# Performance work log

Hardware: AMD Instinct MI355X
Metric: run time of the kernel (lower is better)

## Reference

```python
import jax, jax.numpy as jnp
import numpy as np

B, S, D, H, EXP = 4, 2048, 768, 8, 4
HD = D // H  # head dim = 96
EPS = 1e-5


def layer_norm(x, g, b):
    mu = jnp.mean(x, axis=-1, keepdims=True)
    var = jnp.mean(jnp.square(x - mu), axis=-1, keepdims=True)
    return (x - mu) * jax.lax.rsqrt(var + EPS) * g + b


def setup_inputs() -> dict:
    key = jax.random.key(0)
    ks = jax.random.split(key, 16)
    s = 0.02
    f32 = jnp.float32
    x = jax.random.normal(ks[0], (B, S, D), f32)
    Wq = jax.random.normal(ks[1], (D, D), f32) * s
    bq = jnp.zeros((D,), f32)
    Wk = jax.random.normal(ks[2], (D, D), f32) * s
    bk = jnp.zeros((D,), f32)
    Wv = jax.random.normal(ks[3], (D, D), f32) * s
    bv = jnp.zeros((D,), f32)
    Wo = jax.random.normal(ks[4], (D, D), f32) * s
    bo = jnp.zeros((D,), f32)
    g1 = jnp.ones((D,), f32)
    be1 = jnp.zeros((D,), f32)
    W1 = jax.random.normal(ks[5], (D, D * EXP), f32) * s
    bf1 = jnp.zeros((D * EXP,), f32)
    W2 = jax.random.normal(ks[6], (D * EXP, D), f32) * s
    bf2 = jnp.zeros((D,), f32)
    g2 = jnp.ones((D,), f32)
    be2 = jnp.zeros((D,), f32)
    return dict(x=x, Wq=Wq, bq=bq, Wk=Wk, bk=bk, Wv=Wv, bv=bv, Wo=Wo, bo=bo,
                g1=g1, be1=be1, W1=W1, bf1=bf1, W2=W2, bf2=bf2, g2=g2, be2=be2)


def reference(x, Wq, bq, Wk, bk, Wv, bv, Wo, bo, g1, be1, W1, bf1, W2, bf2, g2, be2):
    scale = HD ** (-0.5)
    # multi-head attention (manual QK^T softmax V)
    q = (x @ Wq + bq).reshape(B, S, H, HD).transpose(0, 2, 1, 3)  # b H s c
    k = (x @ Wk + bk).reshape(B, S, H, HD).transpose(0, 2, 1, 3)
    v = (x @ Wv + bv).reshape(B, S, H, HD).transpose(0, 2, 1, 3)
    scores = jnp.einsum('bhqc,bhkc->bhqk', q, k) * scale
    attn = jax.nn.softmax(scores, axis=-1)
    o = jnp.einsum('bhqk,bhkc->bhqc', attn, v)
    o = o.transpose(0, 2, 1, 3).reshape(B, S, D)
    attn_out = o @ Wo + bo
    # residual + LN
    x1 = layer_norm(attn_out + x, g1, be1)
    # feed-forward with GELU
    h = jax.nn.gelu(x1 @ W1 + bf1)
    ffn_out = h @ W2 + bf2
    # residual + LN
    return layer_norm(ffn_out + x1, g2, be2)
```

## Files before the change

### kernel.cpp

```cpp
#include <hip/hip_runtime.h>
#include <hip/hip_bf16.h>
#include <math.h>
#include <stdint.h>

#define B_    4
#define S_    2048
#define D_    768
#define H_    8
#define HD_   96
#define EXPD_ 3072
#define MSZ   8192

#define QSCALE 0.14724439f
#define M0_    12.0f

typedef __bf16 bf16;
typedef __bf16 bf16x4 __attribute__((ext_vector_type(4)));
typedef __bf16 bf16x8 __attribute__((ext_vector_type(8)));
typedef float  f32x4  __attribute__((ext_vector_type(4)));
typedef float  f32x16 __attribute__((ext_vector_type(16)));

typedef __attribute__((address_space(1))) const uint32_t gu32;
typedef __attribute__((address_space(3))) uint32_t lu32;

__device__ __forceinline__ void async_copy16(const void* g, void* l) {
    __builtin_amdgcn_global_load_lds((gu32*)g, (lu32*)l, 16, 0, 0);
}

template<int N> __device__ __forceinline__ void vm_wait() {
    if constexpr (N == 0)      asm volatile("s_waitcnt vmcnt(0)" ::: "memory");
    else if constexpr (N == 3) asm volatile("s_waitcnt vmcnt(3)" ::: "memory");
    else if constexpr (N == 4) asm volatile("s_waitcnt vmcnt(4)" ::: "memory");
    else static_assert(N == 0 || N == 3 || N == 4, "unsupported vmcnt");
}

__device__ __forceinline__ float gelu_f(float x) {
    float x3 = x * x * x;
    return 0.5f * x * (1.0f + tanhf(0.7978845608028654f * (x + 0.044715f * x3)));
}

__device__ __forceinline__ bool sniff_f32(const void* p) {
    const bf16* pb = (const bf16*)p;
    float v = (float)pb[2 * (threadIdx.x & 63)];
    bool big = !(fabsf(v) < 1000.0f);
    return __any(big) != 0;
}

__device__ __forceinline__ float dynld(const void* p, size_t i, bool f32in) {
    return f32in ? ((const float*)p)[i] : (float)((const bf16*)p)[i];
}

__global__ __launch_bounds__(256) void cast_kernel(
    const void* __restrict__ src, bf16* __restrict__ dst)
{
    const bool f32in = sniff_f32(src);
    size_t i = ((size_t)blockIdx.x * 256 + threadIdx.x) * 8;
    if (f32in) {
        f32x4 a = *(const f32x4*)((const float*)src + i);
        f32x4 b = *(const f32x4*)((const float*)src + i + 4);
        bf16x8 r;
#pragma unroll
        for (int e = 0; e < 4; ++e) { r[e] = (bf16)a[e]; r[e + 4] = (bf16)b[e]; }
        *(bf16x8*)(dst + i) = r;
    } else {
        *(bf16x8*)(dst + i) = *(const bf16x8*)((const bf16*)src + i);
    }
}

#define MODE_QKV  0
#define MODE_RES  1
#define MODE_GELU 2

template<int MODE, bool ADYN, bool RESDYN, int BN>
__global__ __launch_bounds__(256) void gemm2_kernel(
    const void* __restrict__ A, const bf16* __restrict__ Bt,
    const void* __restrict__ b0, const void* __restrict__ b1, const void* __restrict__ b2,
    const void* __restrict__ res, bf16* __restrict__ out,
    int M, int N, int K, int lda, int ldb, int boff, int mstripe,
    const void* __restrict__ sniffp)
{
    constexpr int WN   = BN / 2;
    constexpr int NJ32 = WN / 32;
    constexpr int ABUF = 8192;
    constexpr int BBUF = BN * 64;
    constexpr int BUF  = ABUF + BBUF;
    constexpr int LPH  = 2 + BN / 64;
    __shared__ __align__(16) bf16 Sh[2 * BUF];

    const bool f32in = sniff_f32(sniffp);
    const int tid  = threadIdx.x;
    const int w    = tid >> 6;
    const int lane = tid & 63;
    const int l32  = lane & 31;
    const int kh   = lane >> 5;
    const int wr   = w >> 1, wc = w & 1;

    const int lin  = blockIdx.x;
    const int xcd  = lin & 7;
    const int q    = lin >> 3;
    const int nb   = q / mstripe;
    const int mbin = q - nb * mstripe;
    const int m0   = (xcd * mstripe + mbin) * 128;
    const int n0   = nb * BN;

    const int rsub = lane >> 2;
    const int cswz = (((lane & 3) ^ ((rsub >> 1) & 3))) * 8;
    const int xh   = (l32 >> 1) & 3;

    f32x16 acc[2][NJ32];
#pragma unroll
    for (int i = 0; i < 2; ++i)
#pragma unroll
        for (int j = 0; j < NJ32; ++j)
#pragma unroll
            for (int e = 0; e < 16; ++e) acc[i][j][e] = 0.f;

    const bf16*  Abf = (const bf16*)A;
    const float* Af  = (const float*)A;

    auto stage_half = [&](int k0, int h, int bsel) {
        bf16* As = Sh + bsel * BUF;
        bf16* Bs = As + ABUF;
#pragma unroll
        for (int a = 0; a < 2; ++a) {
            int row = w * 32 + a * 16 + rsub;
            async_copy16(Abf + (size_t)(m0 + row) * lda + k0 + h * 32 + cswz,
                         &As[h * 4096 + (w * 32 + a * 16) * 32]);
        }
#pragma unroll
        for (int a = 0; a < BN / 64; ++a) {
            int row = w * (BN / 4) + a * 16 + rsub;
            async_copy16(Bt + (size_t)(n0 + row) * ldb + k0 + h * 32 + cswz,
                         &Bs[h * (BN * 32) + (w * (BN / 4) + a * 16) * 32]);
        }
    };

    auto compute_half = [&](int hs, int bsel) {
        const bf16* As = Sh + bsel * BUF;
        const bf16* Bs = As + ABUF;
        bf16x8 af[2][2], bfv[NJ32][2];
#pragma unroll
        for (int i = 0; i < 2; ++i)
#pragma unroll
            for (int ks = 0; ks < 2; ++ks)
                af[i][ks] = *(const bf16x8*)(&As[hs * 4096 + (wr * 64 + i * 32 + l32) * 32
                                                + (((ks * 2 + kh) ^ xh) * 8)]);
#pragma unroll
        for (int j = 0; j < NJ32; ++j)
#pragma unroll
            for (int ks = 0; ks < 2; ++ks)
                bfv[j][ks] = *(const bf16x8*)(&Bs[hs * (BN * 32) + (wc * WN + j * 32 + l32) * 32
                                                  + (((ks * 2 + kh) ^ xh) * 8)]);
        asm volatile("s_waitcnt lgkmcnt(0)" ::: "memory");
        __builtin_amdgcn_sched_barrier(0);
        __builtin_amdgcn_s_setprio(1);
#pragma unroll
        for (int i = 0; i < 2; ++i)
#pragma unroll
            for (int j = 0; j < NJ32; ++j)
#pragma unroll
                for (int ks = 0; ks < 2; ++ks)
                    acc[i][j] = __builtin_amdgcn_mfma_f32_32x32x16_bf16(af[i][ks], bfv[j][ks], acc[i][j], 0, 0, 0);
        __builtin_amdgcn_s_setprio(0);
    };

    const int nk = K >> 6;
    if constexpr (ADYN) {
        auto stage = [&](int k0, int bsel) {
            bf16* As = Sh + bsel * BUF;
            bf16* Bs = As + ABUF;
#pragma unroll
            for (int half = 0; half < 2; ++half) {
                if (f32in) {
#pragma unroll
                    for (int a = 0; a < 2; ++a) {
                        const float* sp = Af + (size_t)(m0 + w * 32 + a * 16 + rsub) * lda + k0 + half * 32 + cswz;
                        f32x4 u0 = *(const f32x4*)sp;
                        f32x4 u1 = *(const f32x4*)(sp + 4);
                        bf16x8 v;
#pragma unroll
                        for (int e = 0; e < 4; ++e) { v[e] = (bf16)u0[e]; v[e + 4] = (bf16)u1[e]; }
                        *(bf16x8*)(&As[(size_t)(half * 4096) + (size_t)(w * 32 + a * 16) * 32 + lane * 8]) = v;
                    }
                } else {
#pragma unroll
                    for (int a = 0; a < 2; ++a) {
                        int row = w * 32 + a * 16 + rsub;
                        async_copy16(Abf + (size_t)(m0 + row) * lda + k0 + half * 32 + cswz,
                                     &As[half * 4096 + (w * 32 + a * 16) * 32]);
                    }
                }
#pragma unroll
                for (int a = 0; a < BN / 64; ++a) {
                    int row = w * (BN / 4) + a * 16 + rsub;
                    async_copy16(Bt + (size_t)(n0 + row) * ldb + k0 + half * 32 + cswz,
                                 &Bs[half * (BN * 32) + (w * (BN / 4) + a * 16) * 32]);
                }
            }
        };
        stage(0, 0);
        __syncthreads();
        for (int t = 0; t < nk; ++t) {
            const int cur = t & 1;
            if (t + 1 < nk) stage((t + 1) << 6, cur ^ 1);
            compute_half(0, cur);
            compute_half(1, cur);
            __syncthreads();
        }
    } else {
        stage_half(0, 0, 0);
        stage_half(0, 1, 0);
        vm_wait<LPH>();
        __builtin_amdgcn_s_barrier();
        for (int t = 0; t < nk; ++t) {
            const int cur = t & 1;
            const bool pf = (t + 1 < nk);
#pragma unroll
            for (int h = 0; h < 2; ++h) {
                if (pf) stage_half((t + 1) << 6, h, cur ^ 1);
                compute_half(h, cur);
                if (pf) vm_wait<LPH>(); else vm_wait<0>();
                __builtin_amdgcn_s_barrier();
            }
        }
    }
    __syncthreads();

    if constexpr (MODE == MODE_QKV) {
        bf16* Cw = Sh + w * 2048;
        const int bb = (m0 + wr * 64) >> 11;
#pragma unroll
        for (int j = 0; j < NJ32; ++j) {
            int nbase = n0 + wc * WN + j * 32;
            int which = nbase / D_;
            int n2b   = nbase - which * D_;
            int h     = n2b / HD_;
            int hd0   = n2b - h * HD_;
            const void* bp = which == 0 ? b0 : (which == 1 ? b1 : b2);
            float bval = dynld(bp, n2b + l32, f32in);
            const int bh = bb * H_ + h;
#pragma unroll
            for (int i = 0; i < 2; ++i)
#pragma unroll
                for (int g = 0; g < 16; ++g) {
                    int rr = (g & 3) + 8 * (g >> 2) + 4 * kh;
                    float v = acc[i][j][g] + bval;
                    if (which == 0) v *= QSCALE;
                    Cw[(i * 32 + rr) * 32 + l32] = (bf16)v;
                }
            if (which < 2) {
#pragma unroll
                for (int pass = 0; pass < 4; ++pass) {
                    int row = pass * 16 + (lane >> 2);
                    int c8  = (lane & 3) * 8;
                    bf16x8 cv = *(const bf16x8*)&Cw[row * 32 + c8];
                    int ss = (m0 + wr * 64 + row) & (S_ - 1);
                    size_t dst = (size_t)which * (MSZ * D_) + ((size_t)bh * S_ + ss) * HD_ + hd0 + c8;
                    *(bf16x8*)&out[dst] = cv;
                }
            } else {
                int hd  = hd0 + l32;
                int ss0 = (m0 + wr * 64) & (S_ - 1);
                size_t rowb = (size_t)2 * (MSZ * D_) + ((size_t)bh * HD_ + hd) * S_ + ss0 + kh * 32;
#pragma unroll
                for (int oct = 0; oct < 4; ++oct) {
                    bf16x8 cv;
#pragma unroll
                    for (int e = 0; e < 8; ++e)
                        cv[e] = Cw[(kh * 32 + oct * 8 + e) * 32 + l32];
                    *(bf16x8*)&out[rowb + oct * 8] = cv;
                }
            }
        }
    } else {
        bf16* Cw = Sh + w * 2048;
        for (int j = 0; j < NJ32; ++j) {
            int nl = n0 + wc * WN + j * 32 + l32;
            float bval = boff >= 0 ? dynld(b0, boff + nl, f32in) : 0.f;
#pragma unroll
            for (int i = 0; i < 2; ++i)
#pragma unroll
                for (int g = 0; g < 16; ++g) {
                    int rr = (g & 3) + 8 * (g >> 2) + 4 * kh;
                    float v = acc[i][j][g] + bval;
                    if constexpr (MODE == MODE_GELU) v = gelu_f(v);
                    Cw[(i * 32 + rr) * 32 + l32] = (bf16)v;
                }
#pragma unroll
            for (int pass = 0; pass < 4; ++pass) {
                int row = pass * 16 + (lane >> 2);
                int cc  = (lane & 3) * 8;
                bf16x8 cv = *(const bf16x8*)&Cw[row * 32 + cc];
                int m = m0 + wr * 64 + row;
                int n = n0 + wc * WN + j * 32 + cc;
                size_t off = (size_t)m * N + n;
                if constexpr (MODE == MODE_RES) {
                    bf16x8 o;
                    if (RESDYN && f32in) {
                        f32x4 r0 = *(const f32x4*)((const float*)res + off);
                        f32x4 r1 = *(const f32x4*)((const float*)res + off + 4);
#pragma unroll
                        for (int e = 0; e < 4; ++e) {
                            o[e]     = (bf16)((float)cv[e] + r0[e]);
                            o[e + 4] = (bf16)((float)cv[e + 4] + r1[e]);
                        }
                    } else {
                        bf16x8 rv = *(const bf16x8*)((const bf16*)res + off);
#pragma unroll
                        for (int e = 0; e < 8; ++e) o[e] = (bf16)((float)cv[e] + (float)rv[e]);
                    }
                    *(bf16x8*)&out[off] = o;
                } else {
                    *(bf16x8*)&out[off] = cv;
                }
            }
        }
    }
}

__global__ __launch_bounds__(256, 2) void flash_kernel(
    const bf16* __restrict__ Q, const bf16* __restrict__ Kk,
    const bf16* __restrict__ Vt_g, bf16* __restrict__ ctx)
{
    __shared__ __align__(16) bf16 Ks[64][104];
    __shared__ __align__(16) bf16 Vs[96][72];
    __shared__ __align__(16) bf16 Ps[4][32][72];

    const int tid  = threadIdx.x;
    const int w    = tid >> 6;
    const int lane = tid & 63;
    const int quad = lane >> 4;
    const int l16  = lane & 15;
    const int bh   = blockIdx.x;
    const size_t base = (size_t)bh * S_ * HD_;
    const int q0   = blockIdx.y * 128 + w * 32;

    bf16x8 qf[2][3];
#pragma unroll
    for (int qs = 0; qs < 2; ++qs)
#pragma unroll
        for (int ch = 0; ch < 3; ++ch)
            qf[qs][ch] = *(const bf16x8*)(Q + base + (size_t)(q0 + qs * 16 + l16) * HD_ + ch * 32 + quad * 8);

    f32x4 oacc[2][6];
#pragma unroll
    for (int qs = 0; qs < 2; ++qs)
#pragma unroll
        for (int c = 0; c < 6; ++c) oacc[qs][c] = (f32x4){0.f, 0.f, 0.f, 0.f};
    float lsum[2] = {0.f, 0.f};

    int krow[3], kc8[3], vrow[3], vc8[3];
#pragma unroll
    for (int i = 0; i < 3; ++i) {
        int id = tid + i * 256;
        krow[i] = id / 12; kc8[i] = (id - krow[i] * 12) * 8;
        vrow[i] = id >> 3; vc8[i] = (id & 7) * 8;
    }

    bf16x8 kreg[3], vreg[3];
#pragma unroll
    for (int i = 0; i < 3; ++i) {
        kreg[i] = *(const bf16x8*)(Kk + base + (size_t)krow[i] * HD_ + kc8[i]);
        vreg[i] = *(const bf16x8*)(Vt_g + base + (size_t)vrow[i] * S_ + vc8[i]);
    }
#pragma unroll
    for (int i = 0; i < 3; ++i) {
        *(bf16x8*)(&Ks[krow[i]][kc8[i]]) = kreg[i];
        *(bf16x8*)(&Vs[vrow[i]][vc8[i]]) = vreg[i];
    }
    __syncthreads();

    for (int kv0 = 0; kv0 < S_; kv0 += 64) {
        const bool more = (kv0 + 64) < S_;
        if (more) {
#pragma unroll
            for (int i = 0; i < 3; ++i) {
                kreg[i] = *(const bf16x8*)(Kk + base + (size_t)(kv0 + 64 + krow[i]) * HD_ + kc8[i]);
                vreg[i] = *(const bf16x8*)(Vt_g + base + (size_t)vrow[i] * S_ + kv0 + 64 + vc8[i]);
            }
        }

        f32x4 sacc[2][4];
#pragma unroll
        for (int qs = 0; qs < 2; ++qs)
#pragma unroll
            for (int t = 0; t < 4; ++t)
                sacc[qs][t] = (f32x4){-M0_, -M0_, -M0_, -M0_};
#pragma unroll
        for (int t = 0; t < 4; ++t)
#pragma unroll
            for (int ch = 0; ch < 3; ++ch) {
                bf16x8 kf = *(const bf16x8*)(&Ks[t * 16 + l16][ch * 32 + quad * 8]);
                sacc[0][t] = __builtin_amdgcn_mfma_f32_16x16x32_bf16(kf, qf[0][ch], sacc[0][t], 0, 0, 0);
                sacc[1][t] = __builtin_amdgcn_mfma_f32_16x16x32_bf16(kf, qf[1][ch], sacc[1][t], 0, 0, 0);
            }

#pragma unroll
        for (int qs = 0; qs < 2; ++qs) {
            bf16* prow = &Ps[w][qs * 16 + l16][quad * 4];
#pragma unroll
            for (int t = 0; t < 4; ++t) {
                float p0 = exp2f(sacc[qs][t][0]);
                float p1 = exp2f(sacc[qs][t][1]);
                float p2 = exp2f(sacc[qs][t][2]);
                float p3 = exp2f(sacc[qs][t][3]);
                lsum[qs] += (p0 + p1) + (p2 + p3);
                bf16x4 pv;
                pv[0] = (bf16)p0; pv[1] = (bf16)p1; pv[2] = (bf16)p2; pv[3] = (bf16)p3;
                *(bf16x4*)(prow + t * 16) = pv;
            }
        }

        bf16x8 pf[2][2];
#pragma unroll
        for (int qs = 0; qs < 2; ++qs) {
            pf[qs][0] = *(const bf16x8*)(&Ps[w][qs * 16 + l16][quad * 8]);
            pf[qs][1] = *(const bf16x8*)(&Ps[w][qs * 16 + l16][32 + quad * 8]);
        }
#pragma unroll
        for (int c = 0; c < 6; ++c) {
            bf16x8 vf0 = *(const bf16x8*)(&Vs[c * 16 + l16][quad * 8]);
            bf16x8 vf1 = *(const bf16x8*)(&Vs[c * 16 + l16][32 + quad * 8]);
            oacc[0][c] = __builtin_amdgcn_mfma_f32_16x16x32_bf16(pf[0][0], vf0, oacc[0][c], 0, 0, 0);
            oacc[0][c] = __builtin_amdgcn_mfma_f32_16x16x32_bf16(pf[0][1], vf1, oacc[0][c], 0, 0, 0);
            oacc[1][c] = __builtin_amdgcn_mfma_f32_16x16x32_bf16(pf[1][0], vf0, oacc[1][c], 0, 0, 0);
            oacc[1][c] = __builtin_amdgcn_mfma_f32_16x16x32_bf16(pf[1][1], vf1, oacc[1][c], 0, 0, 0);
        }

        if (more) {
            __syncthreads();
#pragma unroll
            for (int i = 0; i < 3; ++i) {
                *(bf16x8*)(&Ks[krow[i]][kc8[i]]) = kreg[i];
                *(bf16x8*)(&Vs[vrow[i]][vc8[i]]) = vreg[i];
            }
            __syncthreads();
        }
    }

#pragma unroll
    for (int qs = 0; qs < 2; ++qs) {
        lsum[qs] += __shfl_xor(lsum[qs], 16);
        lsum[qs] += __shfl_xor(lsum[qs], 32);
    }
    const int b = bh >> 3, h = bh & 7;
#pragma unroll
    for (int qs = 0; qs < 2; ++qs)
#pragma unroll
        for (int r = 0; r < 4; ++r) {
            float inv = 1.0f / __shfl(lsum[qs], quad * 4 + r);
            int srow = q0 + qs * 16 + quad * 4 + r;
            size_t rowbase = ((size_t)b * S_ + srow) * D_ + h * HD_;
#pragma unroll
            for (int c = 0; c < 6; ++c)
                ctx[rowbase + c * 16 + l16] = (bf16)(oacc[qs][c][r] * inv);
        }
}

template<bool OUTDYN>
__global__ __launch_bounds__(256) void ln_kernel(
    const bf16* __restrict__ in, const void* __restrict__ g, const void* __restrict__ be,
    void* __restrict__ out, const void* __restrict__ sniffp)
{
    const bool f32in = sniff_f32(sniffp);
    const int w = threadIdx.x >> 6, lane = threadIdx.x & 63;
    const int row = blockIdx.x * 4 + w;
    const size_t rbase = (size_t)row * D_ + lane * 12;

    float v[12];
#pragma unroll
    for (int j = 0; j < 3; ++j) {
        bf16x4 t = *(const bf16x4*)(in + rbase + j * 4);
#pragma unroll
        for (int e = 0; e < 4; ++e) v[j * 4 + e] = (float)t[e];
    }
    float sum = 0.f;
#pragma unroll
    for (int j = 0; j < 12; ++j) sum += v[j];
#pragma unroll
    for (int off = 1; off < 64; off <<= 1) sum += __shfl_xor(sum, off);
    float mu = sum * (1.0f / D_);
    float sq = 0.f;
#pragma unroll
    for (int j = 0; j < 12; ++j) { v[j] -= mu; sq += v[j] * v[j]; }
#pragma unroll
    for (int off = 1; off < 64; off <<= 1) sq += __shfl_xor(sq, off);
    float rstd = rsqrtf(sq * (1.0f / D_) + 1e-5f);

    if (OUTDYN && f32in) {
        float* op = (float*)out + rbase;
#pragma unroll
        for (int j = 0; j < 3; ++j) {
            f32x4 t;
#pragma unroll
            for (int e = 0; e < 4; ++e) {
                int c = lane * 12 + j * 4 + e;
                t[e] = v[j * 4 + e] * rstd * dynld(g, c, true) + dynld(be, c, true);
            }
            *(f32x4*)(op + j * 4) = t;
        }
    } else {
        bf16* op = (bf16*)out + rbase;
#pragma unroll
        for (int j = 0; j < 3; ++j) {
            bf16x4 t;
#pragma unroll
            for (int e = 0; e < 4; ++e) {
                int c = lane * 12 + j * 4 + e;
                t[e] = (bf16)(v[j * 4 + e] * rstd * dynld(g, c, f32in) + dynld(be, c, f32in));
            }
            *(bf16x4*)(op + j * 4) = t;
        }
    }
}

__device__ __forceinline__ void transpose_tile(
    const void* __restrict__ src, bf16* __restrict__ dst, int R, int C,
    int r0, int c0, bool f32in)
{
    __shared__ bf16 t[64][65];
    const int tx = threadIdx.x & 63, ty = threadIdx.x >> 6;
#pragma unroll
    for (int i = 0; i < 16; ++i) {
        int rr = ty + i * 4;
        t[rr][tx] = (bf16)dynld(src, (size_t)(r0 + rr) * C + c0 + tx, f32in);
    }
    __syncthreads();
#pragma unroll
    for (int i = 0; i < 16; ++i) {
        int cc = ty + i * 4;
        dst[(size_t)(c0 + cc) * R + r0 + tx] = t[tx][cc];
    }
}

__global__ __launch_bounds__(256) void transpose_qkv_kernel(
    const void* __restrict__ s0, const void* __restrict__ s1, const void* __restrict__ s2,
    bf16* __restrict__ dst)
{
    const void* src = blockIdx.z == 0 ? s0 : (blockIdx.z == 1 ? s1 : s2);
    const bool f32in = sniff_f32(src);
    transpose_tile(src, dst + (size_t)blockIdx.z * D_ * D_, D_, D_,
                   blockIdx.y * 64, blockIdx.x * 64, f32in);
}

__global__ __launch_bounds__(256) void transpose_mlp_kernel(
    const void* __restrict__ s0, const void* __restrict__ s1, const void* __restrict__ s2,
    bf16* __restrict__ dst)
{
    int id = blockIdx.x;
    const void* src;
    int R, C, r, c;
    size_t off;
    if (id < 144)      { src = s0; R = D_;    C = D_;    off = 0;
                         r = id / 12;          c = id % 12; }
    else if (id < 720) { src = s1; R = D_;    C = EXPD_; off = (size_t)D_ * D_;
                         int i = id - 144;     r = i / 48; c = i % 48; }
    else               { src = s2; R = EXPD_; C = D_;    off = (size_t)D_ * D_ + (size_t)D_ * EXPD_;
                         int i = id - 720;     r = i / 12; c = i % 12; }
    const bool f32in = sniff_f32(src);
    transpose_tile(src, dst + off, R, C, r * 64, c * 64, f32in);
}

extern "C" void kernel_launch(void* const* d_in, const int* in_sizes, int n_in,
                              void* d_out, int out_size, void* d_ws, size_t ws_size,
                              hipStream_t stream)
{
    (void)in_sizes; (void)n_in; (void)out_size;
    const void* x   = d_in[0];
    const void* Wq  = d_in[1];
    const void* bq  = d_in[2];
    const void* Wk  = d_in[3];
    const void* bk  = d_in[4];
    const void* Wv  = d_in[5];
    const void* bv  = d_in[6];
    const void* Wo  = d_in[7];
    const void* bo  = d_in[8];
    const void* g1  = d_in[9];
    const void* be1 = d_in[10];
    const void* W1  = d_in[11];
    const void* bf1 = d_in[12];
    const void* W2  = d_in[13];
    const void* bf2 = d_in[14];
    const void* g2  = d_in[15];
    const void* be2 = d_in[16];

    const size_t REG = (size_t)MSZ * D_ * 2;
    char* p = (char*)d_ws;
    bf16* R0 = (bf16*)p;
    bf16* R1 = (bf16*)(p + REG);
    bf16* R2 = (bf16*)(p + 2 * REG);
    bf16* R3 = (bf16*)(p + 3 * REG);
    bf16* R4 = (bf16*)(p + 4 * REG);

    int tier = 0;
    if      (ws_size >= 9 * REG) tier = 3;
    else if (ws_size >= 5 * REG) tier = 1;
    bf16* xb = tier == 3 ? (bf16*)(p + 8 * REG) : R4;

    bf16* qkvT = (bf16*)d_out;
    bf16* ctx  = (bf16*)d_out;
    dim3 blk(256);
    const int MB8 = MSZ / 128 / 8;

    if (tier >= 1) cast_kernel<<<dim3(MSZ * D_ / (256 * 8)), blk, 0, stream>>>(x, xb);

    transpose_qkv_kernel<<<dim3(12, 12, 3), blk, 0, stream>>>(Wq, Wk, Wv, qkvT);

    if (tier >= 1)
        gemm2_kernel<MODE_QKV, false, false, 128><<<dim3(64 * 18), blk, 0, stream>>>(
            xb, qkvT, bq, bk, bv, nullptr, R0, MSZ, 2304, D_, D_, D_, 0, MB8, Wq);
    else
        gemm2_kernel<MODE_QKV, true, false, 128><<<dim3(64 * 18), blk, 0, stream>>>(
            x, qkvT, bq, bk, bv, nullptr, R0, MSZ, 2304, D_, D_, D_, 0, MB8, Wq);

    flash_kernel<<<dim3(B_ * H_, S_ / 128), dim3(256), 0, stream>>>(R0, R1, R2, ctx);

    bf16* WoT = R1;
    bf16* W1T = WoT + (size_t)D_ * D_;
    bf16* W2T = W1T + (size_t)D_ * EXPD_;
    transpose_mlp_kernel<<<dim3(1296), blk, 0, stream>>>(Wo, W1, W2, WoT);

    if (tier >= 1)
        gemm2_kernel<MODE_RES, false, false, 64><<<dim3(64 * 12), blk, 0, stream>>>(
            ctx, WoT, bo, nullptr, nullptr, xb, R3, MSZ, D_, D_, D_, D_, 0, MB8, Wq);
    else
        gemm2_kernel<MODE_RES, false, true, 64><<<dim3(64 * 12), blk, 0, stream>>>(
            ctx, WoT, bo, nullptr, nullptr, x, R3, MSZ, D_, D_, D_, D_, 0, MB8, Wq);

    bf16* x1b = R0;
    ln_kernel<false><<<dim3(MSZ / 4), blk, 0, stream>>>(R3, g1, be1, x1b, Wq);

    bf16* y2b;
    if (tier == 3) {
        bf16* hb = R4;
        y2b = R3;
        gemm2_kernel<MODE_GELU, false, false, 128><<<dim3(64 * 24), blk, 0, stream>>>(
            x1b, W1T, bf1, nullptr, nullptr, nullptr, hb, MSZ, EXPD_, D_, D_, D_, 0, MB8, Wq);
        gemm2_kernel<MODE_RES, false, false, 64><<<dim3(64 * 12), blk, 0, stream>>>(
            hb, W2T, bf2, nullptr, nullptr, x1b, y2b, MSZ, D_, EXPD_, EXPD_, EXPD_, 0, MB8, Wq);
    } else if (tier == 1) {
        bf16* hb = R2;
        y2b = R4;
        gemm2_kernel<MODE_GELU, false, false, 128><<<dim3(64 * 12), blk, 0, stream>>>(
            x1b, W1T, bf1, nullptr, nullptr, nullptr, hb, MSZ, 1536, D_, D_, D_, 0, MB8, Wq);
        gemm2_kernel<MODE_RES, false, false, 64><<<dim3(64 * 12), blk, 0, stream>>>(
            hb, W2T, bf2, nullptr, nullptr, x1b, y2b, MSZ, D_, 1536, 1536, EXPD_, 0, MB8, Wq);
        gemm2_kernel<MODE_GELU, false, false, 128><<<dim3(64 * 12), blk, 0, stream>>>(
            x1b, W1T + (size_t)1536 * D_, bf1, nullptr, nullptr, nullptr, hb, MSZ, 1536, D_, D_, D_, 1536, MB8, Wq);
        gemm2_kernel<MODE_RES, false, false, 64><<<dim3(64 * 12), blk, 0, stream>>>(
            hb, W2T + 1536, nullptr, nullptr, nullptr, y2b, y2b, MSZ, D_, 1536, 1536, EXPD_, -1, MB8, Wq);
    } else {
        bf16* hb = R3;
        y2b = R2;
        const int CH = 2048;
        for (int c0 = 0; c0 < MSZ; c0 += CH) {
            const bf16* x1c = x1b + (size_t)c0 * D_;
            gemm2_kernel<MODE_GELU, false, false, 128><<<dim3(16 * 24), blk, 0, stream>>>(
                x1c, W1T, bf1, nullptr, nullptr, nullptr, hb, CH, EXPD_, D_, D_, D_, 0, 2, Wq);
            gemm2_kernel<MODE_RES, false, false, 64><<<dim3(16 * 12), blk, 0, stream>>>(
                hb, W2T, bf2, nullptr, nullptr, x1c, y2b + (size_t)c0 * D_, CH, D_, EXPD_, EXPD_, EXPD_, 0, 2, Wq);
        }
    }

    ln_kernel<true><<<dim3(MSZ / 4), blk, 0, stream>>>(y2b, g2, be2, d_out, Wq);
}
```

Baseline: 449.9 us.

## Shrink GEMM K-tile to 32 and simplify double-buffered pipeline

Halves the per-stage K depth from 64 to 32, which halves LDS use per buffer. The two-half staging scheme becomes one stage per iteration, with a wait-then-barrier before compute and a barrier after it. Row assignment for the cooperative copies is reshuffled to interleave warps by 16-row groups. The aim is higher occupancy and simpler scheduling, at the cost of twice as many loop iterations and barriers per K and less MFMA work between synchronisations.

```diff
diff --git a/kernel.cpp b/kernel.cpp
--- a/kernel.cpp
+++ b/kernel.cpp
@@ -81,8 +81,8 @@
 {
     constexpr int WN   = BN / 2;
     constexpr int NJ32 = WN / 32;
-    constexpr int ABUF = 8192;
-    constexpr int BBUF = BN * 64;
+    constexpr int ABUF = 4096;
+    constexpr int BBUF = BN * 32;
     constexpr int BUF  = ABUF + BBUF;
     constexpr int LPH  = 2 + BN / 64;
     __shared__ __align__(16) bf16 Sh[2 * BUF];
@@ -118,24 +118,24 @@
     const bf16*  Abf = (const bf16*)A;
     const float* Af  = (const float*)A;
 
-    auto stage_half = [&](int k0, int h, int bsel) {
+    auto stage = [&](int k0, int bsel) {
         bf16* As = Sh + bsel * BUF;
         bf16* Bs = As + ABUF;
 #pragma unroll
-        for (int a = 0; a < 2; ++a) {
-            int row = w * 32 + a * 16 + rsub;
-            async_copy16(Abf + (size_t)(m0 + row) * lda + k0 + h * 32 + cswz,
-                         &As[h * 4096 + (w * 32 + a * 16) * 32]);
-        }
-#pragma unroll
-        for (int a = 0; a < BN / 64; ++a) {
-            int row = w * (BN / 4) + a * 16 + rsub;
-            async_copy16(Bt + (size_t)(n0 + row) * ldb + k0 + h * 32 + cswz,
-                         &Bs[h * (BN * 32) + (w * (BN / 4) + a * 16) * 32]);
+        for (int p = 0; p < 2; ++p) {
+            int row = p * 64 + w * 16;
+            async_copy16(Abf + (size_t)(m0 + row + rsub) * lda + k0 + cswz,
+                         &As[row * 32]);
+        }
+#pragma unroll
+        for (int p = 0; p < BN / 64; ++p) {
+            int row = p * 64 + w * 16;
+            async_copy16(Bt + (size_t)(n0 + row + rsub) * ldb + k0 + cswz,
+                         &Bs[row * 32]);
         }
     };
 
-    auto compute_half = [&](int hs, int bsel) {
+    auto compute = [&](int bsel) {
         const bf16* As = Sh + bsel * BUF;
         const bf16* Bs = As + ABUF;
         bf16x8 af[2][2], bfv[NJ32][2];
@@ -143,13 +143,13 @@
         for (int i = 0; i < 2; ++i)
 #pragma unroll
             for (int ks = 0; ks < 2; ++ks)
-                af[i][ks] = *(const bf16x8*)(&As[hs * 4096 + (wr * 64 + i * 32 + l32) * 32
+                af[i][ks] = *(const bf16x8*)(&As[(wr * 64 + i * 32 + l32) * 32
                                                 + (((ks * 2 + kh) ^ xh) * 8)]);
 #pragma unroll
         for (int j = 0; j < NJ32; ++j)
 #pragma unroll
             for (int ks = 0; ks < 2; ++ks)
-                bfv[j][ks] = *(const bf16x8*)(&Bs[hs * (BN * 32) + (wc * WN + j * 32 + l32) * 32
+                bfv[j][ks] = *(const bf16x8*)(&Bs[(wc * WN + j * 32 + l32) * 32
                                                   + (((ks * 2 + kh) ^ xh) * 8)]);
         asm volatile("s_waitcnt lgkmcnt(0)" ::: "memory");
         __builtin_amdgcn_sched_barrier(0);
@@ -164,64 +164,55 @@
         __builtin_amdgcn_s_setprio(0);
     };
 
-    const int nk = K >> 6;
+    const int nk = K >> 5;
     if constexpr (ADYN) {
-        auto stage = [&](int k0, int bsel) {
+        auto stage_adyn = [&](int k0, int bsel) {
             bf16* As = Sh + bsel * BUF;
             bf16* Bs = As + ABUF;
-#pragma unroll
-            for (int half = 0; half < 2; ++half) {
-                if (f32in) {
-#pragma unroll
-                    for (int a = 0; a < 2; ++a) {
-                        const float* sp = Af + (size_t)(m0 + w * 32 + a * 16 + rsub) * lda + k0 + half * 32 + cswz;
-                        f32x4 u0 = *(const f32x4*)sp;
-                        f32x4 u1 = *(const f32x4*)(sp + 4);
-                        bf16x8 v;
-#pragma unroll
-                        for (int e = 0; e < 4; ++e) { v[e] = (bf16)u0[e]; v[e + 4] = (bf16)u1[e]; }
-                        *(bf16x8*)(&As[(size_t)(half * 4096) + (size_t)(w * 32 + a * 16) * 32 + lane * 8]) = v;
-                    }
-                } else {
-#pragma unroll
-                    for (int a = 0; a < 2; ++a) {
-                        int row = w * 32 + a * 16 + rsub;
-                        async_copy16(Abf + (size_t)(m0 + row) * lda + k0 + half * 32 + cswz,
-                                     &As[half * 4096 + (w * 32 + a * 16) * 32]);
-                    }
+            if (f32in) {
+#pragma unroll
+                for (int p = 0; p < 2; ++p) {
+                    int row = p * 64 + w * 16 + rsub;
+                    const float* sp = Af + (size_t)(m0 + row) * lda + k0 + cswz;
+                    f32x4 u0 = *(const f32x4*)sp;
+                    f32x4 u1 = *(const f32x4*)(sp + 4);
+                    bf16x8 v;
+#pragma unroll
+                    for (int e = 0; e < 4; ++e) { v[e] = (bf16)u0[e]; v[e + 4] = (bf16)u1[e]; }
+                    *(bf16x8*)(&As[row * 32 + (lane & 3) * 8]) = v;
                 }
-#pragma unroll
-                for (int a = 0; a < BN / 64; ++a) {
-                    int row = w * (BN / 4) + a * 16 + rsub;
-                    async_copy16(Bt + (size_t)(n0 + row) * ldb + k0 + half * 32 + cswz,
-                                 &Bs[half * (BN * 32) + (w * (BN / 4) + a * 16) * 32]);
+            } else {
+#pragma unroll
+                for (int p = 0; p < 2; ++p) {
+                    int row = p * 64 + w * 16;
+                    async_copy16(Abf + (size_t)(m0 + row + rsub) * lda + k0 + cswz,
+                                 &As[row * 32]);
                 }
             }
+#pragma unroll
+            for (int p = 0; p < BN / 64; ++p) {
+                int row = p * 64 + w * 16;
+                async_copy16(Bt + (size_t)(n0 + row + rsub) * ldb + k0 + cswz,
+                             &Bs[row * 32]);
+            }
         };
-        stage(0, 0);
+        stage_adyn(0, 0);
         __syncthreads();
         for (int t = 0; t < nk; ++t) {
             const int cur = t & 1;
-            if (t + 1 < nk) stage((t + 1) << 6, cur ^ 1);
-            compute_half(0, cur);
-            compute_half(1, cur);
+            if (t + 1 < nk) stage_adyn((t + 1) << 5, cur ^ 1);
+            compute(cur);
             __syncthreads();
         }
     } else {
-        stage_half(0, 0, 0);
-        stage_half(0, 1, 0);
-        vm_wait<LPH>();
-        __builtin_amdgcn_s_barrier();
+        stage(0, 0);
         for (int t = 0; t < nk; ++t) {
             const int cur = t & 1;
-            const bool pf = (t + 1 < nk);
-#pragma unroll
-            for (int h = 0; h < 2; ++h) {
-                if (pf) stage_half((t + 1) << 6, h, cur ^ 1);
-                compute_half(h, cur);
-                if (pf) vm_wait<LPH>(); else vm_wait<0>();
-                __builtin_amdgcn_s_barrier();
-            }
+            if (t + 1 < nk) { stage((t + 1) << 5, cur ^ 1); vm_wait<LPH>(); }
+            else            { vm_wait<0>(); }
+            __builtin_amdgcn_s_barrier();
+            compute(cur);
+            __builtin_amdgcn_s_barrier();
         }
     }
     __syncthreads();
```

Measured after the change: 438.5 us. -2.5%, faster.
